# Optimization experiments

Hardware: AMD Instinct MI355X
Metric: run time of the kernel (lower is better)

## Reference

```python
import jax, jax.numpy as jnp
import numpy as np

GROUP_SIZE = 128


def setup_inputs() -> dict:
    key = jax.random.key(0)
    k1, k2, k3 = jax.random.split(key, 3)
    B, S, IN, OUT = 4, 8192, 1024, 1024
    x = jax.random.normal(k1, (B, S, IN), dtype=jnp.float32)
    weight = jax.random.normal(k2, (OUT, IN), dtype=jnp.float32) * 0.02
    bias = jax.random.normal(k3, (OUT,), dtype=jnp.float32) * 0.01
    return {"x": x, "weight": weight, "bias": bias}


def reference(x, weight, bias):
    """Quantized int8 path: quantize() + _forward_int8 of OneBitLinear.

    - weights binarized to +/-1 int8 (sign, with 0 -> -1, matching
      sign().clamp(min=0) bit packing then 2*bit-1)
    - per-group weight scales = group absmax, stored fp16 (as in quantize())
    - activations dynamically quantized per-token to int8
    - int32-accumulated GEMM, rescaled by x_scale * mean group scale per row
    """
    out_f, in_f = weight.shape
    ng = in_f // GROUP_SIZE
    w_g = weight.reshape(out_f, ng, GROUP_SIZE)
    # per-group absmax scales, cast fp16 -> fp32 to mimic fp16 storage
    scales = jnp.maximum(jnp.max(jnp.abs(w_g), axis=-1), 1e-8)
    scales = scales.astype(jnp.float16).astype(jnp.float32)  # [O, ng]
    # +/-1 int8 weights (sign>0 -> +1, else -1; zero maps to -1 like the packer)
    w_int8 = jnp.where(weight > 0, 1, -1).astype(jnp.int8)  # [O, I]

    # dynamic per-token activation quantization
    x_f = x.reshape(-1, in_f)  # [BT, I]
    x_scale = jnp.maximum(jnp.max(jnp.abs(x_f), axis=1, keepdims=True), 1e-8) / 127.0
    x_int8 = jnp.clip(jnp.round(x_f / x_scale), -128, 127).astype(jnp.int8)

    # int8 GEMM with int32 accumulation
    out_i32 = jnp.matmul(
        x_int8.astype(jnp.int32), w_int8.T.astype(jnp.int32)
    )  # [BT, O]

    w_scale_per_row = jnp.mean(scales, axis=1)  # [O]
    out_f32 = out_i32.astype(jnp.float32) * x_scale * w_scale_per_row[None, :]
    out_f32 = out_f32 + bias[None, :]
    return out_f32.reshape(*x.shape[:-1], out_f)
```

## Files before the change

### kernel.cpp

```cpp
#include <hip/hip_runtime.h>
#include <hip/hip_fp16.h>

#define K_DIM 1024
#define N_DIM 1024

typedef int v4i __attribute__((ext_vector_type(4)));

__device__ __forceinline__ void async_load16(const void* g, void* l) {
    __builtin_amdgcn_global_load_lds(
        (const __attribute__((address_space(1))) unsigned int*)g,
        (__attribute__((address_space(3))) unsigned int*)l,
        16, 0, 0);
}

#define BAR() do { asm volatile("" ::: "memory"); \
                   __builtin_amdgcn_s_barrier();  \
                   asm volatile("" ::: "memory"); } while (0)

__global__ __launch_bounds__(256) void prep_quant(const float* __restrict__ w,
                                                  const float* __restrict__ x,
                                                  signed char* __restrict__ wq,
                                                  float* __restrict__ wscale,
                                                  signed char* __restrict__ xq,
                                                  float* __restrict__ xs) {
    const int lane = threadIdx.x & 63;
    if (blockIdx.x < 256) {
        const int row = blockIdx.x * 4 + (threadIdx.x >> 6);
        const float4* wr = (const float4*)(w + (size_t)row * K_DIM);
        float4 v[4];
#pragma unroll
        for (int j = 0; j < 4; ++j) v[j] = wr[lane * 4 + j];

        float g = 0.f;
#pragma unroll
        for (int j = 0; j < 4; ++j) {
            g = fmaxf(g, fabsf(v[j].x)); g = fmaxf(g, fabsf(v[j].y));
            g = fmaxf(g, fabsf(v[j].z)); g = fmaxf(g, fabsf(v[j].w));
        }
        g = fmaxf(g, __shfl_xor(g, 1, 64));
        g = fmaxf(g, __shfl_xor(g, 2, 64));
        g = fmaxf(g, __shfl_xor(g, 4, 64));
        const float s = __half2float(__float2half(fmaxf(g, 1e-8f)));
        float t = s;
        t += __shfl_xor(t, 8, 64);
        t += __shfl_xor(t, 16, 64);
        t += __shfl_xor(t, 32, 64);
        if (lane == 0) wscale[row] = t * 0.125f;

        int pk[4];
#pragma unroll
        for (int j = 0; j < 4; ++j) {
            const int b0 = (v[j].x > 0.f) ? 1 : -1;
            const int b1 = (v[j].y > 0.f) ? 1 : -1;
            const int b2 = (v[j].z > 0.f) ? 1 : -1;
            const int b3 = (v[j].w > 0.f) ? 1 : -1;
            pk[j] = (b0 & 255) | ((b1 & 255) << 8) | ((b2 & 255) << 16) | (b3 << 24);
        }
        *(int4*)(wq + (size_t)row * K_DIM + lane * 16) = make_int4(pk[0], pk[1], pk[2], pk[3]);
    } else {
        const int row = (blockIdx.x - 256) * 4 + (threadIdx.x >> 6);
        const float4* xr = (const float4*)(x + (size_t)row * K_DIM);
        float4 v[4];
#pragma unroll
        for (int j = 0; j < 4; ++j) v[j] = xr[lane * 4 + j];

        float am = 0.f;
#pragma unroll
        for (int j = 0; j < 4; ++j) {
            am = fmaxf(am, fabsf(v[j].x)); am = fmaxf(am, fabsf(v[j].y));
            am = fmaxf(am, fabsf(v[j].z)); am = fmaxf(am, fabsf(v[j].w));
        }
#pragma unroll
        for (int off = 32; off >= 1; off >>= 1) am = fmaxf(am, __shfl_xor(am, off, 64));
        const float scale = fmaxf(am, 1e-8f) / 127.f;
        const float inv   = 1.0f / scale;

        int pk[4];
#pragma unroll
        for (int j = 0; j < 4; ++j) {
            const int b0 = (int)fminf(fmaxf(rintf(v[j].x * inv), -128.f), 127.f);
            const int b1 = (int)fminf(fmaxf(rintf(v[j].y * inv), -128.f), 127.f);
            const int b2 = (int)fminf(fmaxf(rintf(v[j].z * inv), -128.f), 127.f);
            const int b3 = (int)fminf(fmaxf(rintf(v[j].w * inv), -128.f), 127.f);
            pk[j] = (b0 & 255) | ((b1 & 255) << 8) | ((b2 & 255) << 16) | (b3 << 24);
        }
        *(int4*)(xq + (size_t)row * K_DIM + lane * 16) = make_int4(pk[0], pk[1], pk[2], pk[3]);
        if (lane == 0) xs[row] = scale;
    }
}

__global__ __launch_bounds__(256, 4) void gemm_i8(const signed char* __restrict__ A,
                                                  const signed char* __restrict__ Bw,
                                                  const float* __restrict__ xs,
                                                  const float* __restrict__ wscale,
                                                  const float* __restrict__ bias,
                                                  float* __restrict__ out) {
    __shared__ __align__(16) signed char As[2][128 * 64];
    __shared__ __align__(16) signed char Bs[2][128 * 64];

    const int tid  = threadIdx.x;
    const int lane = tid & 63;
    const int wave = tid >> 6;
    const int wm = wave >> 1;
    const int wn = wave & 1;

    const int bid = blockIdx.x;
    const int xcd = bid & 7;
    const int q   = bid >> 3;
    const int mT  = xcd * 32 + (q >> 3);
    const int nT  = q & 7;
    const size_t mBase = (size_t)mT * 128;
    const int    nBase = nT * 128;

    const int srow = tid >> 2;
    const int scol = ((tid & 3) ^ (srow & 3)) * 16;
    const int soff = tid * 16;
    const signed char* Ag = A  + (mBase + srow) * K_DIM + scol;
    const signed char* Bg = Bw + (size_t)(nBase + srow) * K_DIM + scol;

#define STAGE(b, kt) do {                                                \
        const int _ko = (kt) * 64;                                       \
        async_load16(Ag + _ko,                      As[b] + soff);       \
        async_load16(Ag + (size_t)64 * K_DIM + _ko, As[b] + 4096 + soff);\
        async_load16(Bg + _ko,                      Bs[b] + soff);       \
        async_load16(Bg + (size_t)64 * K_DIM + _ko, Bs[b] + 4096 + soff);\
    } while (0)

    v4i acc[4][4] = {};
    const int r16 = lane & 15;
    const int g   = lane >> 4;
    const int co  = (g ^ (r16 & 3)) * 16;

    STAGE(0, 0);

    for (int t = 0; t < 16; ++t) {
        asm volatile("s_waitcnt vmcnt(0)" ::: "memory");
        BAR();
        if (t < 15) STAGE((t + 1) & 1, t + 1);

        const signed char* Ab = As[t & 1];
        const signed char* Bb = Bs[t & 1];
        v4i af[4], bf[4];
#pragma unroll
        for (int mf = 0; mf < 4; ++mf)
            af[mf] = *(const v4i*)(Ab + ((wm * 64 + mf * 16 + r16) << 6) + co);
#pragma unroll
        for (int nf = 0; nf < 4; ++nf)
            bf[nf] = *(const v4i*)(Bb + ((wn * 64 + nf * 16 + r16) << 6) + co);

#pragma unroll
        for (int mf = 0; mf < 4; ++mf)
#pragma unroll
            for (int nf = 0; nf < 4; ++nf)
                acc[mf][nf] = __builtin_amdgcn_mfma_i32_16x16x64_i8(
                    af[mf], bf[nf], acc[mf][nf], 0, 0, 0);

        __builtin_amdgcn_sched_barrier(0);
        asm volatile("s_waitcnt lgkmcnt(0)" ::: "memory");
    }
#undef STAGE

    const int cc = r16;
    const int rq = (lane >> 4) * 4;
    float xsr[4][4];
#pragma unroll
    for (int mf = 0; mf < 4; ++mf)
#pragma unroll
        for (int i = 0; i < 4; ++i)
            xsr[mf][i] = xs[mBase + wm * 64 + mf * 16 + rq + i];

#pragma unroll
    for (int nf = 0; nf < 4; ++nf) {
        const int col   = nBase + wn * 64 + nf * 16 + cc;
        const float wsc = wscale[col];
        const float bb  = bias[col];
#pragma unroll
        for (int mf = 0; mf < 4; ++mf) {
#pragma unroll
            for (int i = 0; i < 4; ++i) {
                const size_t row = mBase + wm * 64 + mf * 16 + rq + i;
                out[row * N_DIM + col] = (float)acc[mf][nf][i] * xsr[mf][i] * wsc + bb;
            }
        }
    }
}

extern "C" void kernel_launch(void* const* d_in, const int* in_sizes, int n_in,
                              void* d_out, int out_size, void* d_ws, size_t ws_size,
                              hipStream_t stream) {
    const float* x    = (const float*)d_in[0];
    const float* w    = (const float*)d_in[1];
    const float* bias = (const float*)d_in[2];
    float* out = (float*)d_out;

    const int BT = in_sizes[0] / K_DIM;

    char* ws = (char*)d_ws;
    signed char* xq     = (signed char*)ws;
    float*       xs     = (float*)(ws + (size_t)BT * K_DIM);
    signed char* wq     = (signed char*)(ws + (size_t)BT * K_DIM + (size_t)BT * 4);
    float*       wscale = (float*)((char*)wq + (size_t)N_DIM * K_DIM);

    prep_quant<<<256 + BT / 4, 256, 0, stream>>>(w, x, wq, wscale, xq, xs);
    gemm_i8<<<(BT / 128) * (N_DIM / 128), 256, 0, stream>>>(xq, wq, xs, wscale, bias, out);
}
```

Before: 275.4 us.

## Fuse quantization and int8 GEMM into one cooperative persistent kernel

New measurement: 621.8 us. 126% more time.

```diff
diff --git a/kernel.cpp b/kernel.cpp
--- a/kernel.cpp
+++ b/kernel.cpp
@@ -1,5 +1,8 @@
 #include <hip/hip_runtime.h>
 #include <hip/hip_fp16.h>
+#include <hip/hip_cooperative_groups.h>
+
+namespace cg = cooperative_groups;
 
 #define K_DIM 1024
 #define N_DIM 1024
@@ -16,6 +19,190 @@
 #define BAR() do { asm volatile("" ::: "memory"); \
                    __builtin_amdgcn_s_barrier();  \
                    asm volatile("" ::: "memory"); } while (0)
+
+__global__ __launch_bounds__(256, 4) void fused(const float* __restrict__ x,
+                                                const float* __restrict__ w,
+                                                const float* __restrict__ bias,
+                                                signed char* __restrict__ xq,
+                                                float* __restrict__ xs,
+                                                signed char* __restrict__ wq,
+                                                float* __restrict__ wscale,
+                                                float* __restrict__ out) {
+    __shared__ __align__(16) signed char As[2][128 * 64];
+    __shared__ __align__(16) signed char Bs[2][128 * 64];
+
+    const int tid  = threadIdx.x;
+    const int lane = tid & 63;
+    const int wid  = tid >> 6;
+
+    if (wid == 0) {
+        const int row = blockIdx.x;
+        const float4* wr = (const float4*)(w + (size_t)row * K_DIM);
+        float4 v[4];
+#pragma unroll
+        for (int j = 0; j < 4; ++j) v[j] = wr[lane * 4 + j];
+        float g = 0.f;
+#pragma unroll
+        for (int j = 0; j < 4; ++j) {
+            g = fmaxf(g, fabsf(v[j].x)); g = fmaxf(g, fabsf(v[j].y));
+            g = fmaxf(g, fabsf(v[j].z)); g = fmaxf(g, fabsf(v[j].w));
+        }
+        g = fmaxf(g, __shfl_xor(g, 1, 64));
+        g = fmaxf(g, __shfl_xor(g, 2, 64));
+        g = fmaxf(g, __shfl_xor(g, 4, 64));
+        const float s = __half2float(__float2half(fmaxf(g, 1e-8f)));
+        float t = s;
+        t += __shfl_xor(t, 8, 64);
+        t += __shfl_xor(t, 16, 64);
+        t += __shfl_xor(t, 32, 64);
+        if (lane == 0) wscale[row] = t * 0.125f;
+        int pk[4];
+#pragma unroll
+        for (int j = 0; j < 4; ++j) {
+            const int b0 = (v[j].x > 0.f) ? 1 : -1;
+            const int b1 = (v[j].y > 0.f) ? 1 : -1;
+            const int b2 = (v[j].z > 0.f) ? 1 : -1;
+            const int b3 = (v[j].w > 0.f) ? 1 : -1;
+            pk[j] = (b0 & 255) | ((b1 & 255) << 8) | ((b2 & 255) << 16) | (b3 << 24);
+        }
+        *(int4*)(wq + (size_t)row * K_DIM + lane * 16) = make_int4(pk[0], pk[1], pk[2], pk[3]);
+    }
+
+    {
+        const int rbase = blockIdx.x * 32 + wid * 8;
+        for (int pr = 0; pr < 4; ++pr) {
+            const int r0 = rbase + pr * 2;
+            const float4* x0 = (const float4*)(x + (size_t)r0 * K_DIM);
+            const float4* x1 = (const float4*)(x + (size_t)(r0 + 1) * K_DIM);
+            float4 va[4], vb[4];
+#pragma unroll
+            for (int j = 0; j < 4; ++j) va[j] = x0[lane * 4 + j];
+#pragma unroll
+            for (int j = 0; j < 4; ++j) vb[j] = x1[lane * 4 + j];
+
+            float ama = 0.f, amb = 0.f;
+#pragma unroll
+            for (int j = 0; j < 4; ++j) {
+                ama = fmaxf(ama, fabsf(va[j].x)); ama = fmaxf(ama, fabsf(va[j].y));
+                ama = fmaxf(ama, fabsf(va[j].z)); ama = fmaxf(ama, fabsf(va[j].w));
+                amb = fmaxf(amb, fabsf(vb[j].x)); amb = fmaxf(amb, fabsf(vb[j].y));
+                amb = fmaxf(amb, fabsf(vb[j].z)); amb = fmaxf(amb, fabsf(vb[j].w));
+            }
+#pragma unroll
+            for (int off = 32; off >= 1; off >>= 1) {
+                ama = fmaxf(ama, __shfl_xor(ama, off, 64));
+                amb = fmaxf(amb, __shfl_xor(amb, off, 64));
+            }
+            const float sa = fmaxf(ama, 1e-8f) / 127.f, ia = 1.0f / sa;
+            const float sb = fmaxf(amb, 1e-8f) / 127.f, ib = 1.0f / sb;
+            int pa[4], pb[4];
+#pragma unroll
+            for (int j = 0; j < 4; ++j) {
+                int b0 = (int)fminf(fmaxf(rintf(va[j].x * ia), -128.f), 127.f);
+                int b1 = (int)fminf(fmaxf(rintf(va[j].y * ia), -128.f), 127.f);
+                int b2 = (int)fminf(fmaxf(rintf(va[j].z * ia), -128.f), 127.f);
+                int b3 = (int)fminf(fmaxf(rintf(va[j].w * ia), -128.f), 127.f);
+                pa[j] = (b0 & 255) | ((b1 & 255) << 8) | ((b2 & 255) << 16) | (b3 << 24);
+                b0 = (int)fminf(fmaxf(rintf(vb[j].x * ib), -128.f), 127.f);
+                b1 = (int)fminf(fmaxf(rintf(vb[j].y * ib), -128.f), 127.f);
+                b2 = (int)fminf(fmaxf(rintf(vb[j].z * ib), -128.f), 127.f);
+                b3 = (int)fminf(fmaxf(rintf(vb[j].w * ib), -128.f), 127.f);
+                pb[j] = (b0 & 255) | ((b1 & 255) << 8) | ((b2 & 255) << 16) | (b3 << 24);
+            }
+            *(int4*)(xq + (size_t)r0 * K_DIM + lane * 16)       = make_int4(pa[0], pa[1], pa[2], pa[3]);
+            *(int4*)(xq + (size_t)(r0 + 1) * K_DIM + lane * 16) = make_int4(pb[0], pb[1], pb[2], pb[3]);
+            if (lane == 0) { xs[r0] = sa; xs[r0 + 1] = sb; }
+        }
+    }
+
+    __threadfence();
+    cg::this_grid().sync();
+
+    const int wave = wid;
+    const int wm = wave >> 1;
+    const int wn = wave & 1;
+
+    const int xcd = blockIdx.x & 7;
+    const int u   = blockIdx.x >> 3;
+    const int mT  = xcd * 32 + (u >> 2);
+    const size_t mBase = (size_t)mT * 128;
+
+    const int srow = tid >> 2;
+    const int scol = ((tid & 3) ^ (srow & 3)) * 16;
+    const int soff = tid * 16;
+    const signed char* Ag = xq + (mBase + srow) * K_DIM + scol;
+
+    const int r16 = lane & 15;
+    const int g   = lane >> 4;
+    const int co  = (g ^ (r16 & 3)) * 16;
+    const int rq  = g * 4;
+
+    for (int j = 0; j < 2; ++j) {
+        const int nT    = (u & 3) + 4 * j;
+        const int nBase = nT * 128;
+        const signed char* Bg = wq + (size_t)(nBase + srow) * K_DIM + scol;
+
+#define STAGE(b, kt) do {                                                \
+        const int _ko = (kt) * 64;                                       \
+        async_load16(Ag + _ko,                      As[b] + soff);       \
+        async_load16(Ag + (size_t)64 * K_DIM + _ko, As[b] + 4096 + soff);\
+        async_load16(Bg + _ko,                      Bs[b] + soff);       \
+        async_load16(Bg + (size_t)64 * K_DIM + _ko, Bs[b] + 4096 + soff);\
+    } while (0)
+
+        v4i acc[4][4] = {};
+        STAGE(0, 0);
+
+        for (int t = 0; t < 16; ++t) {
+            asm volatile("s_waitcnt vmcnt(0)" ::: "memory");
+            BAR();
+            if (t < 15) STAGE((t + 1) & 1, t + 1);
+
+            const signed char* Ab = As[t & 1];
+            const signed char* Bb = Bs[t & 1];
+            v4i af[4], bf[4];
+#pragma unroll
+            for (int mf = 0; mf < 4; ++mf)
+                af[mf] = *(const v4i*)(Ab + ((wm * 64 + mf * 16 + r16) << 6) + co);
+#pragma unroll
+            for (int nf = 0; nf < 4; ++nf)
+                bf[nf] = *(const v4i*)(Bb + ((wn * 64 + nf * 16 + r16) << 6) + co);
+
+#pragma unroll
+            for (int mf = 0; mf < 4; ++mf)
+#pragma unroll
+                for (int nf = 0; nf < 4; ++nf)
+                    acc[mf][nf] = __builtin_amdgcn_mfma_i32_16x16x64_i8(
+                        af[mf], bf[nf], acc[mf][nf], 0, 0, 0);
+
+            __builtin_amdgcn_sched_barrier(0);
+            asm volatile("s_waitcnt lgkmcnt(0)" ::: "memory");
+        }
+#undef STAGE
+
+        float xsr[4][4];
+#pragma unroll
+        for (int mf = 0; mf < 4; ++mf)
+#pragma unroll
+            for (int i = 0; i < 4; ++i)
+                xsr[mf][i] = xs[mBase + wm * 64 + mf * 16 + rq + i];
+
+#pragma unroll
+        for (int nf = 0; nf < 4; ++nf) {
+            const int col   = nBase + wn * 64 + nf * 16 + r16;
+            const float wsc = wscale[col];
+            const float bb  = bias[col];
+#pragma unroll
+            for (int mf = 0; mf < 4; ++mf) {
+#pragma unroll
+                for (int i = 0; i < 4; ++i) {
+                    const size_t row = mBase + wm * 64 + mf * 16 + rq + i;
+                    out[row * N_DIM + col] = (float)acc[mf][nf][i] * xsr[mf][i] * wsc + bb;
+                }
+            }
+        }
+    }
+}
 
 __global__ __launch_bounds__(256) void prep_quant(const float* __restrict__ w,
                                                   const float* __restrict__ x,
@@ -30,7 +217,6 @@
         float4 v[4];
 #pragma unroll
         for (int j = 0; j < 4; ++j) v[j] = wr[lane * 4 + j];
-
         float g = 0.f;
 #pragma unroll
         for (int j = 0; j < 4; ++j) {
@@ -46,7 +232,6 @@
         t += __shfl_xor(t, 16, 64);
         t += __shfl_xor(t, 32, 64);
         if (lane == 0) wscale[row] = t * 0.125f;
-
         int pk[4];
 #pragma unroll
         for (int j = 0; j < 4; ++j) {
@@ -63,7 +248,6 @@
         float4 v[4];
 #pragma unroll
         for (int j = 0; j < 4; ++j) v[j] = xr[lane * 4 + j];
-
         float am = 0.f;
 #pragma unroll
         for (int j = 0; j < 4; ++j) {
@@ -74,7 +258,6 @@
         for (int off = 32; off >= 1; off >>= 1) am = fmaxf(am, __shfl_xor(am, off, 64));
         const float scale = fmaxf(am, 1e-8f) / 127.f;
         const float inv   = 1.0f / scale;
-
         int pk[4];
 #pragma unroll
         for (int j = 0; j < 4; ++j) {
@@ -97,13 +280,10 @@
                                                   float* __restrict__ out) {
     __shared__ __align__(16) signed char As[2][128 * 64];
     __shared__ __align__(16) signed char Bs[2][128 * 64];
-
     const int tid  = threadIdx.x;
     const int lane = tid & 63;
     const int wave = tid >> 6;
-    const int wm = wave >> 1;
-    const int wn = wave & 1;
-
+    const int wm = wave >> 1, wn = wave & 1;
     const int bid = blockIdx.x;
     const int xcd = bid & 7;
     const int q   = bid >> 3;
@@ -111,13 +291,11 @@
     const int nT  = q & 7;
     const size_t mBase = (size_t)mT * 128;
     const int    nBase = nT * 128;
-
     const int srow = tid >> 2;
     const int scol = ((tid & 3) ^ (srow & 3)) * 16;
     const int soff = tid * 16;
     const signed char* Ag = A  + (mBase + srow) * K_DIM + scol;
     const signed char* Bg = Bw + (size_t)(nBase + srow) * K_DIM + scol;
-
 #define STAGE(b, kt) do {                                                \
         const int _ko = (kt) * 64;                                       \
         async_load16(Ag + _ko,                      As[b] + soff);       \
@@ -125,19 +303,15 @@
         async_load16(Bg + _ko,                      Bs[b] + soff);       \
         async_load16(Bg + (size_t)64 * K_DIM + _ko, Bs[b] + 4096 + soff);\
     } while (0)
-
     v4i acc[4][4] = {};
     const int r16 = lane & 15;
     const int g   = lane >> 4;
     const int co  = (g ^ (r16 & 3)) * 16;
-
     STAGE(0, 0);
-
     for (int t = 0; t < 16; ++t) {
         asm volatile("s_waitcnt vmcnt(0)" ::: "memory");
         BAR();
         if (t < 15) STAGE((t + 1) & 1, t + 1);
-
         const signed char* Ab = As[t & 1];
         const signed char* Bb = Bs[t & 1];
         v4i af[4], bf[4];
@@ -147,19 +321,16 @@
 #pragma unroll
         for (int nf = 0; nf < 4; ++nf)
             bf[nf] = *(const v4i*)(Bb + ((wn * 64 + nf * 16 + r16) << 6) + co);
-
 #pragma unroll
         for (int mf = 0; mf < 4; ++mf)
 #pragma unroll
             for (int nf = 0; nf < 4; ++nf)
                 acc[mf][nf] = __builtin_amdgcn_mfma_i32_16x16x64_i8(
                     af[mf], bf[nf], acc[mf][nf], 0, 0, 0);
-
         __builtin_amdgcn_sched_barrier(0);
         asm volatile("s_waitcnt lgkmcnt(0)" ::: "memory");
     }
 #undef STAGE
-
     const int cc = r16;
     const int rq = (lane >> 4) * 4;
     float xsr[4][4];
@@ -168,7 +339,6 @@
 #pragma unroll
         for (int i = 0; i < 4; ++i)
             xsr[mf][i] = xs[mBase + wm * 64 + mf * 16 + rq + i];
-
 #pragma unroll
     for (int nf = 0; nf < 4; ++nf) {
         const int col   = nBase + wn * 64 + nf * 16 + cc;
@@ -201,6 +371,12 @@
     signed char* wq     = (signed char*)(ws + (size_t)BT * K_DIM + (size_t)BT * 4);
     float*       wscale = (float*)((char*)wq + (size_t)N_DIM * K_DIM);
 
-    prep_quant<<<256 + BT / 4, 256, 0, stream>>>(w, x, wq, wscale, xq, xs);
-    gemm_i8<<<(BT / 128) * (N_DIM / 128), 256, 0, stream>>>(xq, wq, xs, wscale, bias, out);
-}
+    void* args[8] = { (void*)&x, (void*)&w, (void*)&bias, (void*)&xq,
+                      (void*)&xs, (void*)&wq, (void*)&wscale, (void*)&out };
+    hipError_t e = hipLaunchCooperativeKernel(reinterpret_cast<void*>(fused),
+                                              dim3(1024), dim3(256), args, 0, stream);
+    if (e != hipSuccess) {
+        prep_quant<<<256 + BT / 4, 256, 0, stream>>>(w, x, wq, wscale, xq, xs);
+        gemm_i8<<<(BT / 128) * (N_DIM / 128), 256, 0, stream>>>(xq, wq, xs, wscale, bias, out);
+    }
+}
```
